# Kernel tuning notes

Measured on AMD Instinct MI355X. Metric: run time of the kernel, lower is better.

## Reference

```python
import jax, jax.numpy as jnp
import numpy as np

B, N, D, E, FF_MULT = 2, 1024, 1024, 8, 4
H = D * FF_MULT


def setup_inputs() -> dict:
    key = jax.random.key(0)
    k = jax.random.split(key, 6)
    tokens = jax.random.normal(k[0], (B, N, D), dtype=jnp.float32)
    # uniform(0,1): strictly positive -> every expert processes every token
    dispatch_weights = jax.random.uniform(k[1], (B, N, E), dtype=jnp.float32)
    combine_weights = jax.random.uniform(k[2], (B, N, E), dtype=jnp.float32)
    # per-expert SwiGLU params, stacked on leading expert axis.
    # stored pre-transposed: y = x @ W  (torch Linear weight is [out,in])
    xavier_dh = np.sqrt(2.0 / (D + H))
    Wg = jax.random.normal(k[3], (E, D, H), dtype=jnp.float32) * xavier_dh
    Wv = jax.random.normal(k[4], (E, D, H), dtype=jnp.float32) * xavier_dh
    Wo = jax.random.normal(k[5], (E, H, D), dtype=jnp.float32) * (0.02 * xavier_dh)
    scale = jnp.full((E,), 1.0 / E, dtype=jnp.float32)  # output_scale init 1/E
    return {"tokens": tokens, "dispatch_weights": dispatch_weights,
            "combine_weights": combine_weights, "Wg": Wg, "Wv": Wv,
            "Wo": Wo, "scale": scale}


def reference(tokens, dispatch_weights, combine_weights, Wg, Wv, Wo, scale):
    b, n, d = tokens.shape
    x = tokens.reshape(b * n, d)                      # (T, D)
    disp = dispatch_weights.reshape(b * n, E)         # (T, E)
    comb = combine_weights.reshape(b * n, E)          # (T, E)
    # SwiGLU FFN for all experts at once (dense grouped GEMM)
    gate = jax.nn.gelu(jnp.einsum('td,edh->teh', x, Wg), approximate=False)
    value = jnp.einsum('td,edh->teh', x, Wv)
    expert_out = jnp.einsum('teh,ehd->ted', gate * value, Wo)  # (T, E, D)
    expert_out = expert_out * scale[None, :, None]
    # combine: weight by combine_weights where dispatched (dispatch > 0)
    w = jnp.where(disp > 0, comb, 0.0)                # (T, E)
    output = jnp.einsum('ted,te->td', expert_out, w)
    return output.reshape(b, n, d)
```

## Files before the change

kernel.cpp:

```cpp
#include <hip/hip_runtime.h>
#include <math.h>

#define T_TOK 2048
#define DDIM 1024
#define HDIM 4096
#define NEXP 8
#define NPRIME 8192
#define KTOT (NEXP * HDIM)
#define NSPLIT 8

typedef unsigned short u16;
typedef __attribute__((ext_vector_type(4))) float f32x4;
typedef __attribute__((ext_vector_type(8))) __bf16 bf16x8;
typedef __attribute__((ext_vector_type(8))) unsigned short u16x8;
typedef __attribute__((ext_vector_type(4))) unsigned short u16x4;

__device__ __forceinline__ u16 f2bf(float f) {
  unsigned int u = __builtin_bit_cast(unsigned int, f);
  u += 0x7fffu + ((u >> 16) & 1u);
  return (u16)(u >> 16);
}

__device__ __forceinline__ void stage16(const u16* g, u16* l) {
  __builtin_amdgcn_global_load_lds((__attribute__((address_space(1))) void*)g,
                                   (__attribute__((address_space(3))) void*)l,
                                   16, 0, 0);
}

__global__ void cvt_x_kernel(const float* __restrict__ x, u16* __restrict__ xb) {
  int i = (blockIdx.x * 256 + threadIdx.x) * 8;
  float4 a = *(const float4*)(x + i);
  float4 b = *(const float4*)(x + i + 4);
  u16x8 o;
  o[0] = f2bf(a.x); o[1] = f2bf(a.y); o[2] = f2bf(a.z); o[3] = f2bf(a.w);
  o[4] = f2bf(b.x); o[5] = f2bf(b.y); o[6] = f2bf(b.z); o[7] = f2bf(b.w);
  *(u16x8*)(xb + i) = o;
}

__global__ void transpose_all_kernel(const float* __restrict__ Wg,
                                     const float* __restrict__ Wv,
                                     const float* __restrict__ Wo,
                                     u16* __restrict__ wgvT, u16* __restrict__ woT2) {
  __shared__ float lds[64][65];
  const int bid = blockIdx.x;
  const int e = bid / 3072;
  const int r = bid % 3072;
  const int which = r >> 10;
  const int tt = r & 1023;
  const float* src; int R, C;
  if (which == 2) { src = Wo + (size_t)e * HDIM * DDIM; R = HDIM; C = DDIM; }
  else            { src = (which ? Wv : Wg) + (size_t)e * DDIM * HDIM; R = DDIM; C = HDIM; }
  const int nrt = R >> 6;
  const int r0 = (tt % nrt) << 6, c0 = (tt / nrt) << 6;
  const int tid = threadIdx.x;
#pragma unroll
  for (int i = 0; i < 4; ++i) {
    int f4 = tid + 256 * i;
    int row = f4 >> 4, c4 = (f4 & 15) << 2;
    float4 v = *(const float4*)(src + (size_t)(r0 + row) * C + c0 + c4);
    lds[row][c4] = v.x; lds[row][c4 + 1] = v.y; lds[row][c4 + 2] = v.z; lds[row][c4 + 3] = v.w;
  }
  __syncthreads();
#pragma unroll
  for (int i = 0; i < 4; ++i) {
    int f4 = tid + 256 * i;
    int cc = f4 >> 4, r4 = (f4 & 15) << 2;
    u16x4 o;
    o[0] = f2bf(lds[r4][cc]);     o[1] = f2bf(lds[r4 + 1][cc]);
    o[2] = f2bf(lds[r4 + 2][cc]); o[3] = f2bf(lds[r4 + 3][cc]);
    u16* dst;
    if (which == 2) {
      dst = woT2 + (size_t)(c0 + cc) * KTOT + e * HDIM + r0 + r4;
    } else {
      int h = c0 + cc;
      int rowp = ((h >> 4) << 5) + which * 16 + (h & 15);
      dst = wgvT + (size_t)e * NPRIME * DDIM + (size_t)rowp * DDIM + r0 + r4;
    }
    *(u16x4*)dst = o;
  }
}


template<int KS>
__device__ __forceinline__ void gemm_loop(const u16* Ab, const u16* Bb,
                                          int Am0, int Bn0, int kbase, int NT,
                                          u16* lds, int tid, f32x4 (&acc)[8][4]) {
  const int lane = tid & 63;
  const int wave = tid >> 6;
  const int wm = wave >> 2, wn = wave & 3;
  const int l15 = lane & 15, lkq = lane >> 4;

  const int sl = tid & 7, rw = tid >> 3;
  const int slx = (sl ^ (rw & 7)) << 3;
  const int rb = (rw & 31) + ((rw >> 5) << 6);
  const u16* pA = Ab + (size_t)(Am0 + rw) * KS + kbase + slx;
  const u16* pB = Bb + (size_t)(Bn0 + rb) * KS + kbase + slx;
  const int dA = rw * 64 + sl * 8;
  const int dB = 16384 + rb * 64 + sl * 8;

  auto slotp = [&](int t) -> u16* { return lds + (t & 1) * 32768; };
  auto SA0 = [&](int t) { u16* sp = slotp(t); const int k = t << 6;
    stage16(pA + k, sp + dA);
    stage16(pA + (size_t)128 * KS + k, sp + dA + 8192); };
  auto SA1 = [&](int t) { u16* sp = slotp(t); const int k = t << 6;
    stage16(pA + (size_t)64 * KS + k, sp + dA + 4096);
    stage16(pA + (size_t)192 * KS + k, sp + dA + 12288); };
  auto SB0 = [&](int t) { u16* sp = slotp(t); const int k = t << 6;
    stage16(pB + k, sp + dB);
    stage16(pB + (size_t)128 * KS + k, sp + dB + 8192); };
  auto SB1 = [&](int t) { u16* sp = slotp(t); const int k = t << 6;
    stage16(pB + (size_t)32 * KS + k, sp + dB + 2048);
    stage16(pB + (size_t)160 * KS + k, sp + dB + 10240); };

  const int swz0 = (lkq ^ (l15 & 7)) << 3;
  const int swz1 = ((4 | lkq) ^ (l15 & 7)) << 3;
  const int arow = (wm * 128 + l15) * 64;
  const int brow = 16384 + (wn * 64 + l15) * 64;
  const int a0 = arow + swz0, a1 = arow + swz1;
  const int b0 = brow + swz0, b1 = brow + swz1;

  SA0(0); SB0(0); SB1(0); SA1(0);
  asm volatile("s_waitcnt vmcnt(0)" ::: "memory");
  __builtin_amdgcn_s_barrier();

#pragma unroll 1
  for (int t = 0; t < NT; ++t) {
    const u16* s = slotp(t);
    const int tp1 = (t + 1 < NT) ? t + 1 : NT - 1;
    bf16x8 af[8], bfr[4];

#pragma unroll
    for (int mf = 0; mf < 8; ++mf) af[mf] = *(const bf16x8*)(s + a0 + mf * 1024);
#pragma unroll
    for (int nf = 0; nf < 4; ++nf) bfr[nf] = *(const bf16x8*)(s + b0 + nf * 1024);
    SA0(tp1); SB0(tp1);
    __builtin_amdgcn_s_setprio(1);
#pragma unroll
    for (int mf = 0; mf < 8; ++mf)
#pragma unroll
      for (int nf = 0; nf < 4; ++nf)
        acc[mf][nf] = __builtin_amdgcn_mfma_f32_16x16x32_bf16(af[mf], bfr[nf], acc[mf][nf], 0, 0, 0);
    __builtin_amdgcn_s_setprio(0);

#pragma unroll
    for (int mf = 0; mf < 8; ++mf) af[mf] = *(const bf16x8*)(s + a1 + mf * 1024);
#pragma unroll
    for (int nf = 0; nf < 4; ++nf) bfr[nf] = *(const bf16x8*)(s + b1 + nf * 1024);
    SB1(tp1); SA1(tp1);
    __builtin_amdgcn_s_setprio(1);
#pragma unroll
    for (int mf = 0; mf < 8; ++mf)
#pragma unroll
      for (int nf = 0; nf < 4; ++nf)
        acc[mf][nf] = __builtin_amdgcn_mfma_f32_16x16x32_bf16(af[mf], bfr[nf], acc[mf][nf], 0, 0, 0);
    __builtin_amdgcn_s_setprio(0);

    asm volatile("s_waitcnt vmcnt(0)" ::: "memory");
    __builtin_amdgcn_s_barrier();
  }
}

__global__ void __launch_bounds__(512, 2)
gemm_gv_kernel(const u16* __restrict__ xb, const u16* __restrict__ wgvT,
               const float* __restrict__ disp, const float* __restrict__ comb,
               const float* __restrict__ scale, u16* __restrict__ h) {
  __shared__ u16 lds[65536];

  const int bid = blockIdx.x;
  const int wg = (bid & 7) * 256 + (bid >> 3);
  const int e  = wg >> 8;
  const int rr = wg & 255;
  const int nt = rr >> 3;
  const int mt = rr & 7;

  const int tid = threadIdx.x;
  const int lane = tid & 63;
  const int wave = tid >> 6;
  const int wm = wave >> 2, wn = wave & 3;
  const int l15 = lane & 15, lkq = lane >> 4;

  const u16* Bb = wgvT + (size_t)e * NPRIME * DDIM;
  const int Am0 = mt * 256;
  const int Bn0 = nt * 256;

  f32x4 acc[8][4] = {};
  gemm_loop<DDIM>(xb, Bb, Am0, Bn0, 0, DDIM / 64, lds, tid, acc);

  const float s_e = scale[e];
  const int hbase = nt * 128 + wn * 32;
#pragma unroll
  for (int a = 0; a < 8; ++a) {
#pragma unroll
    for (int r = 0; r < 4; ++r) {
      const int t = Am0 + wm * 128 + a * 16 + lkq * 4 + r;
      const float dv = disp[t * NEXP + e];
      const float cv = comb[t * NEXP + e];
      const float s = (dv > 0.0f) ? cv * s_e : 0.0f;
#pragma unroll
      for (int jj = 0; jj < 2; ++jj) {
        const float g = acc[a][2 * jj][r];
        const float v = acc[a][2 * jj + 1][r];
        const float ge = 0.5f * g * (1.0f + erff(g * 0.70710678f));
        h[(size_t)t * KTOT + e * HDIM + hbase + jj * 16 + l15] = f2bf(ge * v * s);
      }
    }
  }
}

__global__ void __launch_bounds__(512, 2)
gemm_out_kernel(const u16* __restrict__ hb, const u16* __restrict__ woT2,
                float* __restrict__ P) {
  __shared__ u16 lds[65536];

  const int bid = blockIdx.x;
  const int wg = (bid & 7) * 32 + (bid >> 3);
  const int kz = wg >> 5;
  const int rr = wg & 31;
  const int nt = rr >> 3;
  const int mt = rr & 7;

  const int tid = threadIdx.x;
  const int lane = tid & 63;
  const int wave = tid >> 6;
  const int wm = wave >> 2, wn = wave & 3;
  const int l15 = lane & 15, lkq = lane >> 4;

  const int Am0 = mt * 256;
  const int Bn0 = nt * 256;
  const int kbase = kz * (KTOT / NSPLIT);

  f32x4 acc[8][4] = {};
  gemm_loop<KTOT>(hb, woT2, Am0, Bn0, kbase, (KTOT / NSPLIT) / 64, lds, tid, acc);

  float* Pp = P + (size_t)kz * (T_TOK * DDIM);
#pragma unroll
  for (int a = 0; a < 8; ++a) {
#pragma unroll
    for (int r = 0; r < 4; ++r) {
      const int t = Am0 + wm * 128 + a * 16 + lkq * 4 + r;
#pragma unroll
      for (int nf = 0; nf < 4; ++nf)
        Pp[(size_t)t * DDIM + Bn0 + wn * 64 + nf * 16 + l15] = acc[a][nf][r];
    }
  }
}

__global__ void reduce_out_kernel(const float* __restrict__ P, float* __restrict__ out) {
  int i = blockIdx.x * 256 + threadIdx.x;
  float4 a = ((const float4*)P)[i];
#pragma unroll
  for (int s = 1; s < NSPLIT; ++s) {
    float4 b = ((const float4*)P)[i + s * (T_TOK * DDIM / 4)];
    a.x += b.x; a.y += b.y; a.z += b.z; a.w += b.w;
  }
  ((float4*)out)[i] = a;
}

extern "C" void kernel_launch(void* const* d_in, const int* in_sizes, int n_in,
                              void* d_out, int out_size, void* d_ws, size_t ws_size,
                              hipStream_t stream) {
  const float* tokens = (const float*)d_in[0];
  const float* disp   = (const float*)d_in[1];
  const float* comb   = (const float*)d_in[2];
  const float* Wg     = (const float*)d_in[3];
  const float* Wv     = (const float*)d_in[4];
  const float* Wo     = (const float*)d_in[5];
  const float* scale  = (const float*)d_in[6];
  float* out = (float*)d_out;

  char* ws = (char*)d_ws;
  const size_t MB = 1024 * 1024;
  u16* xb    = (u16*)(ws);
  u16* wgvT  = (u16*)(ws + 4   * MB);
  u16* woT2  = (u16*)(ws + 132 * MB);
  u16* hbuf  = (u16*)(ws + 196 * MB);
  float* P   = (float*)(ws + 324 * MB);

  cvt_x_kernel<<<1024, 256, 0, stream>>>(tokens, xb);
  transpose_all_kernel<<<24576, 256, 0, stream>>>(Wg, Wv, Wo, wgvT, woT2);
  gemm_gv_kernel<<<2048, 512, 0, stream>>>(xb, wgvT, disp, comb, scale, hbuf);
  gemm_out_kernel<<<256, 512, 0, stream>>>(hbuf, woT2, P);
  reduce_out_kernel<<<2048, 256, 0, stream>>>(P, out);
}
```

Before: 566.4 us.

## Shrink GEMM block tile to 256x128 with 4 waves and reworked LDS buffering

Both GEMM kernels move from 512-thread blocks computing 256x256 tiles to 256-thread blocks computing 256x128 tiles, doubling the grid sizes. LDS per block is halved. The A tile is single-buffered: its fragments for both k-halves are loaded into registers before a barrier, then the next A tile is staged into the same slot. The B tile is double-buffered. The intent is to let two blocks share a CU and to give the split-K output GEMM more blocks to spread across CUs. The cost is less operand reuse per tile, an extra barrier per iteration, and more A-fragment registers.

```diff
diff --git a/kernel.cpp b/kernel.cpp
--- a/kernel.cpp
+++ b/kernel.cpp
@@ -87,72 +87,70 @@
                                           u16* lds, int tid, f32x4 (&acc)[8][4]) {
   const int lane = tid & 63;
   const int wave = tid >> 6;
-  const int wm = wave >> 2, wn = wave & 3;
+  const int wm = wave >> 1, wn = wave & 1;
   const int l15 = lane & 15, lkq = lane >> 4;
 
-  const int sl = tid & 7, rw = tid >> 3;
-  const int slx = (sl ^ (rw & 7)) << 3;
-  const int rb = (rw & 31) + ((rw >> 5) << 6);
-  const u16* pA = Ab + (size_t)(Am0 + rw) * KS + kbase + slx;
-  const u16* pB = Bb + (size_t)(Bn0 + rb) * KS + kbase + slx;
-  const int dA = rw * 64 + sl * 8;
-  const int dB = 16384 + rb * 64 + sl * 8;
-
-  auto slotp = [&](int t) -> u16* { return lds + (t & 1) * 32768; };
-  auto SA0 = [&](int t) { u16* sp = slotp(t); const int k = t << 6;
-    stage16(pA + k, sp + dA);
-    stage16(pA + (size_t)128 * KS + k, sp + dA + 8192); };
-  auto SA1 = [&](int t) { u16* sp = slotp(t); const int k = t << 6;
-    stage16(pA + (size_t)64 * KS + k, sp + dA + 4096);
-    stage16(pA + (size_t)192 * KS + k, sp + dA + 12288); };
-  auto SB0 = [&](int t) { u16* sp = slotp(t); const int k = t << 6;
-    stage16(pB + k, sp + dB);
-    stage16(pB + (size_t)128 * KS + k, sp + dB + 8192); };
-  auto SB1 = [&](int t) { u16* sp = slotp(t); const int k = t << 6;
-    stage16(pB + (size_t)32 * KS + k, sp + dB + 2048);
-    stage16(pB + (size_t)160 * KS + k, sp + dB + 10240); };
+  const int sl = tid & 7, r0 = tid >> 3;
+  const int slx = (sl ^ (r0 & 7)) << 3;
+  const u16* pA = Ab + (size_t)(Am0 + r0) * KS + kbase + slx;
+  const u16* pB = Bb + (size_t)(Bn0 + r0) * KS + kbase + slx;
+  const int dA0 = r0 * 64 + sl * 8;
+  const int dB0 = r0 * 64 + sl * 8;
 
   const int swz0 = (lkq ^ (l15 & 7)) << 3;
   const int swz1 = ((4 | lkq) ^ (l15 & 7)) << 3;
   const int arow = (wm * 128 + l15) * 64;
-  const int brow = 16384 + (wn * 64 + l15) * 64;
+  const int brow = (wn * 64 + l15) * 64;
   const int a0 = arow + swz0, a1 = arow + swz1;
   const int b0 = brow + swz0, b1 = brow + swz1;
 
-  SA0(0); SB0(0); SB1(0); SA1(0);
+#pragma unroll
+  for (int i = 0; i < 8; ++i) stage16(pA + (size_t)(i * 32) * KS, lds + dA0 + i * 2048);
+#pragma unroll
+  for (int i = 0; i < 4; ++i) stage16(pB + (size_t)(i * 32) * KS, lds + 16384 + dB0 + i * 2048);
   asm volatile("s_waitcnt vmcnt(0)" ::: "memory");
   __builtin_amdgcn_s_barrier();
 
 #pragma unroll 1
   for (int t = 0; t < NT; ++t) {
-    const u16* s = slotp(t);
+    const int bs = 16384 + ((t & 1) << 13);
+    const int bn = 16384 + (((t + 1) & 1) << 13);
     const int tp1 = (t + 1 < NT) ? t + 1 : NT - 1;
-    bf16x8 af[8], bfr[4];
-
-#pragma unroll
-    for (int mf = 0; mf < 8; ++mf) af[mf] = *(const bf16x8*)(s + a0 + mf * 1024);
-#pragma unroll
-    for (int nf = 0; nf < 4; ++nf) bfr[nf] = *(const bf16x8*)(s + b0 + nf * 1024);
-    SA0(tp1); SB0(tp1);
+    const size_t kn = (size_t)(tp1 << 6);
+    bf16x8 af[8][2], bfr[4];
+
+#pragma unroll
+    for (int mf = 0; mf < 8; ++mf) {
+      af[mf][0] = *(const bf16x8*)(lds + a0 + mf * 1024);
+      af[mf][1] = *(const bf16x8*)(lds + a1 + mf * 1024);
+    }
+#pragma unroll
+    for (int nf = 0; nf < 4; ++nf) bfr[nf] = *(const bf16x8*)(lds + bs + b0 + nf * 1024);
+    asm volatile("s_waitcnt lgkmcnt(0)" ::: "memory");
+    __builtin_amdgcn_s_barrier();
+
+#pragma unroll
+    for (int i = 0; i < 8; ++i) stage16(pA + (size_t)(i * 32) * KS + kn, lds + dA0 + i * 2048);
+#pragma unroll
+    for (int i = 0; i < 4; ++i) stage16(pB + (size_t)(i * 32) * KS + kn, lds + bn + dB0 + i * 2048);
+    __builtin_amdgcn_sched_barrier(0);
+
     __builtin_amdgcn_s_setprio(1);
 #pragma unroll
     for (int mf = 0; mf < 8; ++mf)
 #pragma unroll
       for (int nf = 0; nf < 4; ++nf)
-        acc[mf][nf] = __builtin_amdgcn_mfma_f32_16x16x32_bf16(af[mf], bfr[nf], acc[mf][nf], 0, 0, 0);
+        acc[mf][nf] = __builtin_amdgcn_mfma_f32_16x16x32_bf16(af[mf][0], bfr[nf], acc[mf][nf], 0, 0, 0);
     __builtin_amdgcn_s_setprio(0);
 
 #pragma unroll
-    for (int mf = 0; mf < 8; ++mf) af[mf] = *(const bf16x8*)(s + a1 + mf * 1024);
-#pragma unroll
-    for (int nf = 0; nf < 4; ++nf) bfr[nf] = *(const bf16x8*)(s + b1 + nf * 1024);
-    SB1(tp1); SA1(tp1);
+    for (int nf = 0; nf < 4; ++nf) bfr[nf] = *(const bf16x8*)(lds + bs + b1 + nf * 1024);
     __builtin_amdgcn_s_setprio(1);
 #pragma unroll
     for (int mf = 0; mf < 8; ++mf)
 #pragma unroll
       for (int nf = 0; nf < 4; ++nf)
-        acc[mf][nf] = __builtin_amdgcn_mfma_f32_16x16x32_bf16(af[mf], bfr[nf], acc[mf][nf], 0, 0, 0);
+        acc[mf][nf] = __builtin_amdgcn_mfma_f32_16x16x32_bf16(af[mf][1], bfr[nf], acc[mf][nf], 0, 0, 0);
     __builtin_amdgcn_s_setprio(0);
 
     asm volatile("s_waitcnt vmcnt(0)" ::: "memory");
@@ -160,34 +158,34 @@
   }
 }
 
-__global__ void __launch_bounds__(512, 2)
+__global__ void __launch_bounds__(256, 2)
 gemm_gv_kernel(const u16* __restrict__ xb, const u16* __restrict__ wgvT,
                const float* __restrict__ disp, const float* __restrict__ comb,
                const float* __restrict__ scale, u16* __restrict__ h) {
-  __shared__ u16 lds[65536];
+  __shared__ u16 lds[32768];
 
   const int bid = blockIdx.x;
-  const int wg = (bid & 7) * 256 + (bid >> 3);
-  const int e  = wg >> 8;
-  const int rr = wg & 255;
+  const int wg = (bid & 7) * 512 + (bid >> 3);
+  const int e  = wg >> 9;
+  const int rr = wg & 511;
   const int nt = rr >> 3;
   const int mt = rr & 7;
 
   const int tid = threadIdx.x;
   const int lane = tid & 63;
   const int wave = tid >> 6;
-  const int wm = wave >> 2, wn = wave & 3;
+  const int wm = wave >> 1, wn = wave & 1;
   const int l15 = lane & 15, lkq = lane >> 4;
 
   const u16* Bb = wgvT + (size_t)e * NPRIME * DDIM;
   const int Am0 = mt * 256;
-  const int Bn0 = nt * 256;
+  const int Bn0 = nt * 128;
 
   f32x4 acc[8][4] = {};
   gemm_loop<DDIM>(xb, Bb, Am0, Bn0, 0, DDIM / 64, lds, tid, acc);
 
   const float s_e = scale[e];
-  const int hbase = nt * 128 + wn * 32;
+  const int hbase = nt * 64 + wn * 32;
 #pragma unroll
   for (int a = 0; a < 8; ++a) {
 #pragma unroll
@@ -207,26 +205,26 @@
   }
 }
 
-__global__ void __launch_bounds__(512, 2)
+__global__ void __launch_bounds__(256, 2)
 gemm_out_kernel(const u16* __restrict__ hb, const u16* __restrict__ woT2,
                 float* __restrict__ P) {
-  __shared__ u16 lds[65536];
+  __shared__ u16 lds[32768];
 
   const int bid = blockIdx.x;
-  const int wg = (bid & 7) * 32 + (bid >> 3);
-  const int kz = wg >> 5;
-  const int rr = wg & 31;
+  const int wg = (bid & 7) * 64 + (bid >> 3);
+  const int kz = wg >> 6;
+  const int rr = wg & 63;
   const int nt = rr >> 3;
   const int mt = rr & 7;
 
   const int tid = threadIdx.x;
   const int lane = tid & 63;
   const int wave = tid >> 6;
-  const int wm = wave >> 2, wn = wave & 3;
+  const int wm = wave >> 1, wn = wave & 1;
   const int l15 = lane & 15, lkq = lane >> 4;
 
   const int Am0 = mt * 256;
-  const int Bn0 = nt * 256;
+  const int Bn0 = nt * 128;
   const int kbase = kz * (KTOT / NSPLIT);
 
   f32x4 acc[8][4] = {};
@@ -278,7 +276,7 @@
 
   cvt_x_kernel<<<1024, 256, 0, stream>>>(tokens, xb);
   transpose_all_kernel<<<24576, 256, 0, stream>>>(Wg, Wv, Wo, wgvT, woT2);
-  gemm_gv_kernel<<<2048, 512, 0, stream>>>(xb, wgvT, disp, comb, scale, hbuf);
-  gemm_out_kernel<<<256, 512, 0, stream>>>(hbuf, woT2, P);
+  gemm_gv_kernel<<<4096, 256, 0, stream>>>(xb, wgvT, disp, comb, scale, hbuf);
+  gemm_out_kernel<<<512, 256, 0, stream>>>(hbuf, woT2, P);
   reduce_out_kernel<<<2048, 256, 0, stream>>>(P, out);
 }
```

Result: no change. 564.0 us (-0.4%).
